# Kernel tuning notes

Measured on AMD Instinct MI355X. Metric: run time of the kernel, lower is better.

The kernel has to match this reference:

```python
import jax, jax.numpy as jnp
import numpy as np

TAU = 1.0

def setup_inputs() -> dict:
    key = jax.random.key(0)
    k1, k2, k3 = jax.random.split(key, 3)
    B, D, C = 16384, 1024, 1000
    hidden_states = jax.random.normal(k1, (B, D), dtype=jnp.float32)
    prototype_matrix = jax.random.normal(k2, (C, D), dtype=jnp.float32)
    labels = jax.random.randint(k3, (B,), 0, C, dtype=jnp.int64)
    return {"hidden_states": hidden_states, "prototype_matrix": prototype_matrix, "labels": labels}

def reference(hidden_states, prototype_matrix, labels):
    # Per-sample L2 normalize (matches x / x.norm())
    x = hidden_states / jnp.linalg.norm(hidden_states, axis=-1, keepdims=True)  # [B, D]
    # Cosine-similarity logits against class prototypes, scaled by tau=1.0
    logits = jnp.einsum('bd,cd->bc', x, prototype_matrix) / TAU  # [B, C]
    # -log( exp(logit_y) / sum exp(logits) ) == cross-entropy with log_softmax
    logp = jax.nn.log_softmax(logits, axis=-1)
    per_loss = -jnp.take_along_axis(logp, labels[:, None], axis=1)[:, 0]  # [B]
    return jnp.mean(per_loss)  # reduction='mean'
```

## Files before the change

kernel.cpp:

```cpp
#include <hip/hip_runtime.h>
#include <hip/hip_bf16.h>

#define B_ROWS 16384
#define DDIM   1024
#define CCLS   1000
#define CPAD   1024
#define GN     4

typedef __attribute__((ext_vector_type(8))) short  short8;
typedef __attribute__((ext_vector_type(4))) float  f32x4;

static __device__ __forceinline__ unsigned short f2bf(float f) {
    unsigned int u = __float_as_uint(f);
    unsigned int r = 0x7fffu + ((u >> 16) & 1u);
    return (unsigned short)((u + r) >> 16);
}

static __device__ __forceinline__ void gl_lds16(const unsigned short* g, unsigned short* l) {
    __builtin_amdgcn_global_load_lds(
        (const __attribute__((address_space(1))) void*)g,
        (__attribute__((address_space(3))) void*)l, 16, 0, 0);
}

__global__ __launch_bounds__(256) void prep(
        const float* __restrict__ H, const float* __restrict__ P,
        unsigned short* __restrict__ Hb, unsigned short* __restrict__ Pb,
        float* __restrict__ rowscale) {
    const int bid = blockIdx.x;
    const int tid = threadIdx.x;
    const int w   = tid >> 6;
    const int l   = tid & 63;
    if (bid < 2048) {
        #pragma unroll
        for (int p = 0; p < 2; ++p) {
            const int row = bid * 8 + w * 2 + p;
            const float* src = H + (size_t)row * DDIM;
            unsigned short* dst = Hb + (size_t)row * DDIM;
            float ss = 0.f;
            #pragma unroll
            for (int c = 0; c < 4; ++c) {
                const int col = c * 256 + l * 4;
                const float4 v = *reinterpret_cast<const float4*>(src + col);
                ss += v.x*v.x + v.y*v.y + v.z*v.z + v.w*v.w;
                ushort4 o = {f2bf(v.x), f2bf(v.y), f2bf(v.z), f2bf(v.w)};
                *reinterpret_cast<ushort4*>(dst + col) = o;
            }
            #pragma unroll
            for (int mask = 1; mask < 64; mask <<= 1)
                ss += __shfl_xor(ss, mask);
            if (l == 0) rowscale[row] = 1.4426950408889634f * rsqrtf(ss);
        }
    } else {
        const int pb = bid - 2048;
        #pragma unroll 4
        for (int c = 0; c < 32; ++c) {
            const int base = (pb * 8192 + c * 256 + tid) * 4;
            const int row  = base >> 10;
            ushort4 o;
            if (row < CCLS) {
                const float4 v = *reinterpret_cast<const float4*>(P + base);
                o.x = f2bf(v.x); o.y = f2bf(v.y); o.z = f2bf(v.z); o.w = f2bf(v.w);
            } else {
                o.x = o.y = o.z = o.w = 0;
            }
            *reinterpret_cast<ushort4*>(Pb + base) = o;
        }
    }
}

__global__ __launch_bounds__(512, 2) void gemm_ce(
        const unsigned short* __restrict__ Hb,
        const unsigned short* __restrict__ Pb,
        const int* __restrict__ labels,
        const float* __restrict__ rowscale,
        float* __restrict__ psum,
        float* __restrict__ plab) {
    __shared__ unsigned short Alds[2][256 * 64];
    __shared__ unsigned short Blds[2][256 * 64];

    const int orig = blockIdx.x;
    const int wg   = (orig & 7) * 32 + (orig >> 3);
    const int bm   = wg >> 2;
    const int bn   = wg & 3;

    const int tid = threadIdx.x;
    const int w   = tid >> 6;
    const int l   = tid & 63;
    const int lo  = l & 15;
    const int hi  = l >> 4;
    const int wm  = w >> 2;
    const int wn  = w & 3;

    const size_t arow0 = (size_t)bm * 256;
    const size_t brow0 = (size_t)bn * 256;

    const int srow = l >> 3;
    const int scol = ((l & 7) ^ srow) * 8;

#define STAGE(buf_, kt_) do {                                                   \
    _Pragma("unroll")                                                           \
    for (int i_ = 0; i_ < 4; ++i_) {                                            \
        const int trow_ = i_ * 64 + w * 8 + srow;                               \
        gl_lds16(Hb + (arow0 + trow_) * DDIM + (kt_) * 64 + scol,               \
                 &Alds[buf_][i_ * 4096 + w * 512]);                             \
        gl_lds16(Pb + (brow0 + trow_) * DDIM + (kt_) * 64 + scol,               \
                 &Blds[buf_][i_ * 4096 + w * 512]);                             \
    }                                                                           \
} while (0)

    f32x4 acc[8][4];
    #pragma unroll
    for (int m = 0; m < 8; ++m)
        #pragma unroll
        for (int n = 0; n < 4; ++n)
            acc[m][n] = (f32x4){0.f, 0.f, 0.f, 0.f};

    const int swz = (lo & 7) << 4;

    STAGE(0, 0);
    for (int kt = 0; kt < 16; ++kt) {
        const int cur = kt & 1;
        if (kt < 15) {
            STAGE(cur ^ 1, kt + 1);
            asm volatile("s_waitcnt vmcnt(8)" ::: "memory");
        } else {
            asm volatile("s_waitcnt vmcnt(0)" ::: "memory");
        }
        __builtin_amdgcn_s_barrier();
        __builtin_amdgcn_sched_barrier(0);

        const char* Ab = (const char*)&Alds[cur][0];
        const char* Bb = (const char*)&Blds[cur][0];
        #pragma unroll
        for (int kk = 0; kk < 2; ++kk) {
            const int col = ((kk << 6) | (hi << 4)) ^ swz;
            short8 a[8], b[4];
            #pragma unroll
            for (int m = 0; m < 8; ++m)
                a[m] = *reinterpret_cast<const short8*>(
                    Ab + (wm * 128 + m * 16 + lo) * 128 + col);
            #pragma unroll
            for (int n = 0; n < 4; ++n)
                b[n] = *reinterpret_cast<const short8*>(
                    Bb + (wn * 64 + n * 16 + lo) * 128 + col);
            __builtin_amdgcn_s_setprio(1);
            #pragma unroll
            for (int n = 0; n < 4; ++n)
                #pragma unroll
                for (int m = 0; m < 8; ++m)
                    acc[m][n] = __builtin_amdgcn_mfma_f32_16x16x32_bf16(
                        a[m], b[n], acc[m][n], 0, 0, 0);
            __builtin_amdgcn_s_setprio(0);
        }
        __builtin_amdgcn_sched_barrier(0);
        __builtin_amdgcn_s_barrier();
    }
#undef STAGE

    float* red = reinterpret_cast<float*>(&Alds[0][0]);
    #pragma unroll
    for (int m = 0; m < 8; ++m) {
        const int rloc = wm * 128 + m * 16 + hi * 4;
        float rs4[4], s4[4], lb2[4];
        int   lb4[4];
        #pragma unroll
        for (int j = 0; j < 4; ++j) {
            const size_t grow = arow0 + rloc + j;
            rs4[j] = rowscale[grow];
            lb4[j] = labels[grow];
            s4[j]  = 0.f;
            lb2[j] = -1e30f;
        }
        #pragma unroll
        for (int n = 0; n < 4; ++n) {
            const int c = (int)brow0 + wn * 64 + n * 16 + lo;
            const float pen = (c < CCLS) ? 0.f : -1e30f;
            #pragma unroll
            for (int j = 0; j < 4; ++j) {
                const float lg = fmaf(acc[m][n][j], rs4[j], pen);
                lb2[j] = (c == lb4[j]) ? lg : lb2[j];
                s4[j] += exp2f(lg);
            }
        }
        #pragma unroll
        for (int j = 0; j < 4; ++j) {
            #pragma unroll
            for (int mask = 1; mask <= 8; mask <<= 1) {
                s4[j]  += __shfl_xor(s4[j], mask);
                lb2[j]  = fmaxf(lb2[j], __shfl_xor(lb2[j], mask));
            }
            if (lo == 0) {
                const int r = rloc + j;
                red[(r * 4 + wn) * 2 + 0] = s4[j];
                red[(r * 4 + wn) * 2 + 1] = lb2[j];
            }
        }
    }
    __syncthreads();
    if (tid < 256) {
        float st = 0.f, lt = -1e30f;
        #pragma unroll
        for (int q = 0; q < 4; ++q) {
            st += red[(tid * 4 + q) * 2 + 0];
            lt  = fmaxf(lt, red[(tid * 4 + q) * 2 + 1]);
        }
        const size_t grow = arow0 + tid;
        psum[grow * GN + bn] = st;
        plab[grow * GN + bn] = lt;
    }
}

__global__ __launch_bounds__(256) void reduce1(
        const float* __restrict__ psum, const float* __restrict__ plab,
        float* __restrict__ partials) {
    const int tid = threadIdx.x;
    const size_t row = (size_t)blockIdx.x * 256 + tid;
    float st = 0.f, lt = -1e30f;
    #pragma unroll
    for (int g = 0; g < GN; ++g) {
        st += psum[row * GN + g];
        lt  = fmaxf(lt, plab[row * GN + g]);
    }
    float loss = 0.6931471805599453f * (log2f(st) - lt);
    #pragma unroll
    for (int mask = 1; mask < 64; mask <<= 1)
        loss += __shfl_xor(loss, mask);
    __shared__ float wsum[4];
    if ((tid & 63) == 0) wsum[tid >> 6] = loss;
    __syncthreads();
    if (tid == 0)
        partials[blockIdx.x] = wsum[0] + wsum[1] + wsum[2] + wsum[3];
}

__global__ void reduce2(const float* __restrict__ partials, float* __restrict__ out) {
    float v = partials[threadIdx.x];
    #pragma unroll
    for (int mask = 1; mask < 64; mask <<= 1)
        v += __shfl_xor(v, mask);
    if (threadIdx.x == 0) out[0] = v * (1.0f / 16384.0f);
}

extern "C" void kernel_launch(void* const* d_in, const int* in_sizes, int n_in,
                              void* d_out, int out_size, void* d_ws, size_t ws_size,
                              hipStream_t stream) {
    const float* H      = (const float*)d_in[0];
    const float* P      = (const float*)d_in[1];
    const int*   labels = (const int*)d_in[2];
    float* out = (float*)d_out;

    char* wp = (char*)d_ws;
    unsigned short* Hb = (unsigned short*)wp;   wp += (size_t)B_ROWS * DDIM * 2;
    unsigned short* Pb = (unsigned short*)wp;   wp += (size_t)CPAD * DDIM * 2;
    float* rowscale    = (float*)wp;            wp += (size_t)B_ROWS * 4;
    float* psum        = (float*)wp;            wp += (size_t)B_ROWS * GN * 4;
    float* plab        = (float*)wp;            wp += (size_t)B_ROWS * GN * 4;
    float* partials    = (float*)wp;

    prep<<<2080, 256, 0, stream>>>(H, P, Hb, Pb, rowscale);
    gemm_ce<<<(B_ROWS / 256) * GN, 512, 0, stream>>>(Hb, Pb, labels, rowscale, psum, plab);
    reduce1<<<B_ROWS / 256, 256, 0, stream>>>(psum, plab, partials);
    reduce2<<<1, 64, 0, stream>>>(partials, out);
}
```

Before: 74.60 us.

## Interleave quarter-tile LDS reads with staged prefetch and fuse final reductions

The GEMM main loop is split into four phases, each covering a quarter of the output tile. LDS fragment loads and global-to-LDS prefetches for tiles one and two steps ahead are spread across these phases, so memory traffic overlaps the MFMA work instead of running in a separate block. The two trailing reduction kernels become a single one-block kernel with vectorized loads, which removes one launch. The cost is more barriers per k-tile, more complex buffer reuse where a buffer is refilled while still being read, and a serial single-block final reduction.

```diff
diff --git a/kernel.cpp b/kernel.cpp
--- a/kernel.cpp
+++ b/kernel.cpp
@@ -6,6 +6,7 @@
 #define CCLS   1000
 #define CPAD   1024
 #define GN     4
+#define NKT    16
 
 typedef __attribute__((ext_vector_type(8))) short  short8;
 typedef __attribute__((ext_vector_type(4))) float  f32x4;
@@ -97,16 +98,12 @@
     const int srow = l >> 3;
     const int scol = ((l & 7) ^ srow) * 8;
 
-#define STAGE(buf_, kt_) do {                                                   \
-    _Pragma("unroll")                                                           \
-    for (int i_ = 0; i_ < 4; ++i_) {                                            \
-        const int trow_ = i_ * 64 + w * 8 + srow;                               \
-        gl_lds16(Hb + (arow0 + trow_) * DDIM + (kt_) * 64 + scol,               \
-                 &Alds[buf_][i_ * 4096 + w * 512]);                             \
-        gl_lds16(Pb + (brow0 + trow_) * DDIM + (kt_) * 64 + scol,               \
-                 &Blds[buf_][i_ * 4096 + w * 512]);                             \
-    }                                                                           \
-} while (0)
+#define STAGE_A(buf_, t_, q_) gl_lds16(                                         \
+        Hb + (arow0 + (q_) * 64 + w * 8 + srow) * DDIM + (t_) * 64 + scol,      \
+        &Alds[buf_][((q_) * 64 + w * 8) * 64])
+#define STAGE_B(buf_, t_, q_) gl_lds16(                                         \
+        Pb + (brow0 + (q_) * 64 + w * 8 + srow) * DDIM + (t_) * 64 + scol,      \
+        &Blds[buf_][((q_) * 64 + w * 8) * 64])
 
     f32x4 acc[8][4];
     #pragma unroll
@@ -115,47 +112,88 @@
         for (int n = 0; n < 4; ++n)
             acc[m][n] = (f32x4){0.f, 0.f, 0.f, 0.f};
 
-    const int swz = (lo & 7) << 4;
-
-    STAGE(0, 0);
-    for (int kt = 0; kt < 16; ++kt) {
-        const int cur = kt & 1;
-        if (kt < 15) {
-            STAGE(cur ^ 1, kt + 1);
-            asm volatile("s_waitcnt vmcnt(8)" ::: "memory");
-        } else {
-            asm volatile("s_waitcnt vmcnt(0)" ::: "memory");
-        }
-        __builtin_amdgcn_s_barrier();
-        __builtin_amdgcn_sched_barrier(0);
-
-        const char* Ab = (const char*)&Alds[cur][0];
-        const char* Bb = (const char*)&Blds[cur][0];
-        #pragma unroll
-        for (int kk = 0; kk < 2; ++kk) {
-            const int col = ((kk << 6) | (hi << 4)) ^ swz;
-            short8 a[8], b[4];
-            #pragma unroll
-            for (int m = 0; m < 8; ++m)
-                a[m] = *reinterpret_cast<const short8*>(
-                    Ab + (wm * 128 + m * 16 + lo) * 128 + col);
-            #pragma unroll
-            for (int n = 0; n < 4; ++n)
-                b[n] = *reinterpret_cast<const short8*>(
-                    Bb + (wn * 64 + n * 16 + lo) * 128 + col);
-            __builtin_amdgcn_s_setprio(1);
-            #pragma unroll
-            for (int n = 0; n < 4; ++n)
-                #pragma unroll
-                for (int m = 0; m < 8; ++m)
-                    acc[m][n] = __builtin_amdgcn_mfma_f32_16x16x32_bf16(
-                        a[m], b[n], acc[m][n], 0, 0, 0);
-            __builtin_amdgcn_s_setprio(0);
-        }
-        __builtin_amdgcn_sched_barrier(0);
-        __builtin_amdgcn_s_barrier();
-    }
-#undef STAGE
+    const int swz   = (lo & 7) << 4;
+    const int colk0 = (hi << 4) ^ swz;
+    const int colk1 = (64 | (hi << 4)) ^ swz;
+
+    short8 a[4][2];
+    short8 b[4][2];
+
+#define LDA(base_, mh_) do { _Pragma("unroll")                                  \
+    for (int mi_ = 0; mi_ < 4; ++mi_) {                                         \
+        const int r_ = (wm * 128 + (mh_) * 64 + mi_ * 16 + lo) * 128;           \
+        a[mi_][0] = *reinterpret_cast<const short8*>((base_) + r_ + colk0);     \
+        a[mi_][1] = *reinterpret_cast<const short8*>((base_) + r_ + colk1);     \
+    } } while (0)
+#define LDB(base_, nh_) do { _Pragma("unroll")                                  \
+    for (int ni_ = 0; ni_ < 2; ++ni_) {                                         \
+        const int r_ = (wn * 64 + ((nh_) * 2 + ni_) * 16 + lo) * 128;           \
+        b[(nh_)*2+ni_][0] = *reinterpret_cast<const short8*>((base_) + r_ + colk0); \
+        b[(nh_)*2+ni_][1] = *reinterpret_cast<const short8*>((base_) + r_ + colk1); \
+    } } while (0)
+#define MFMA_Q(mh_, nh_) do { _Pragma("unroll")                                 \
+    for (int kk_ = 0; kk_ < 2; ++kk_) { _Pragma("unroll")                       \
+    for (int ni_ = 0; ni_ < 2; ++ni_) { _Pragma("unroll")                       \
+    for (int mi_ = 0; mi_ < 4; ++mi_) {                                         \
+        acc[(mh_)*4+mi_][(nh_)*2+ni_] = __builtin_amdgcn_mfma_f32_16x16x32_bf16(\
+            a[mi_][kk_], b[(nh_)*2+ni_][kk_], acc[(mh_)*4+mi_][(nh_)*2+ni_],    \
+            0, 0, 0);                                                           \
+    } } } } while (0)
+#define PHASE_TAIL(mh_, nh_)                                                    \
+    __builtin_amdgcn_s_barrier();                                               \
+    asm volatile("s_waitcnt lgkmcnt(0)" ::: "memory");                          \
+    __builtin_amdgcn_sched_barrier(0);                                          \
+    __builtin_amdgcn_s_setprio(1);                                              \
+    MFMA_Q(mh_, nh_);                                                           \
+    __builtin_amdgcn_s_setprio(0);                                              \
+    __builtin_amdgcn_s_barrier()
+
+#define TILE_ITER(p_, t_) do {                                                  \
+    const char* Ab_ = (const char*)&Alds[p_][0];                                \
+    const char* Bb_ = (const char*)&Blds[p_][0];                                \
+                                                                   \
+    LDA(Ab_, 0); LDB(Bb_, 0);                                                   \
+    if ((t_) + 1 < NKT) { STAGE_A((p_) ^ 1, (t_) + 1, 1);                       \
+                          STAGE_A((p_) ^ 1, (t_) + 1, 3); }                     \
+    PHASE_TAIL(0, 0);                                                           \
+                                                                   \
+    LDB(Bb_, 1);                                                                \
+    if ((t_) + 2 < NKT) { STAGE_A(p_, (t_) + 2, 0); STAGE_A(p_, (t_) + 2, 2); } \
+    PHASE_TAIL(0, 1);                                                           \
+                                                                   \
+    LDA(Ab_, 1);                                                                \
+    if ((t_) + 2 < NKT) { STAGE_B(p_, (t_) + 2, 0); STAGE_B(p_, (t_) + 2, 1); } \
+    PHASE_TAIL(1, 0);                                                           \
+                                                                   \
+    if ((t_) + 2 < NKT) { STAGE_B(p_, (t_) + 2, 2); STAGE_B(p_, (t_) + 2, 3);   \
+        asm volatile("s_waitcnt vmcnt(6)" ::: "memory");                        \
+    } else if ((t_) + 1 < NKT) {                                                \
+        asm volatile("s_waitcnt vmcnt(0)" ::: "memory");                        \
+    }                                                                           \
+    PHASE_TAIL(1, 1);                                                           \
+} while (0)
+
+    #pragma unroll
+    for (int q = 0; q < 4; ++q) { STAGE_A(0, 0, q); STAGE_B(0, 0, q); }
+    STAGE_A(1, 1, 0); STAGE_A(1, 1, 2);
+    #pragma unroll
+    for (int q = 0; q < 4; ++q) STAGE_B(1, 1, q);
+    asm volatile("s_waitcnt vmcnt(6)" ::: "memory");
+    __builtin_amdgcn_s_barrier();
+
+    #pragma unroll 1
+    for (int kt2 = 0; kt2 < NKT / 2; ++kt2) {
+        const int t0 = 2 * kt2;
+        TILE_ITER(0, t0);
+        TILE_ITER(1, t0 + 1);
+    }
+#undef TILE_ITER
+#undef PHASE_TAIL
+#undef MFMA_Q
+#undef LDB
+#undef LDA
+#undef STAGE_B
+#undef STAGE_A
 
     float* red = reinterpret_cast<float*>(&Alds[0][0]);
     #pragma unroll
@@ -210,34 +248,33 @@
     }
 }
 
-__global__ __launch_bounds__(256) void reduce1(
+__global__ __launch_bounds__(1024) void reduce_all(
         const float* __restrict__ psum, const float* __restrict__ plab,
-        float* __restrict__ partials) {
+        float* __restrict__ out) {
     const int tid = threadIdx.x;
-    const size_t row = (size_t)blockIdx.x * 256 + tid;
-    float st = 0.f, lt = -1e30f;
-    #pragma unroll
-    for (int g = 0; g < GN; ++g) {
-        st += psum[row * GN + g];
-        lt  = fmaxf(lt, plab[row * GN + g]);
-    }
-    float loss = 0.6931471805599453f * (log2f(st) - lt);
+    float loss = 0.f;
+    #pragma unroll 4
+    for (int i = 0; i < B_ROWS / 1024; ++i) {
+        const int row = i * 1024 + tid;
+        const float4 ps = *reinterpret_cast<const float4*>(psum + (size_t)row * GN);
+        const float4 pl = *reinterpret_cast<const float4*>(plab + (size_t)row * GN);
+        const float st = (ps.x + ps.y) + (ps.z + ps.w);
+        const float lt = fmaxf(fmaxf(pl.x, pl.y), fmaxf(pl.z, pl.w));
+        loss += 0.6931471805599453f * (log2f(st) - lt);
+    }
     #pragma unroll
     for (int mask = 1; mask < 64; mask <<= 1)
         loss += __shfl_xor(loss, mask);
-    __shared__ float wsum[4];
+    __shared__ float wsum[16];
     if ((tid & 63) == 0) wsum[tid >> 6] = loss;
     __syncthreads();
-    if (tid == 0)
-        partials[blockIdx.x] = wsum[0] + wsum[1] + wsum[2] + wsum[3];
-}
-
-__global__ void reduce2(const float* __restrict__ partials, float* __restrict__ out) {
-    float v = partials[threadIdx.x];
-    #pragma unroll
-    for (int mask = 1; mask < 64; mask <<= 1)
-        v += __shfl_xor(v, mask);
-    if (threadIdx.x == 0) out[0] = v * (1.0f / 16384.0f);
+    if (tid < 64) {
+        float v = (tid < 16) ? wsum[tid] : 0.f;
+        #pragma unroll
+        for (int mask = 1; mask < 16; mask <<= 1)
+            v += __shfl_xor(v, mask);
+        if (tid == 0) out[0] = v * (1.0f / 16384.0f);
+    }
 }
 
 extern "C" void kernel_launch(void* const* d_in, const int* in_sizes, int n_in,
@@ -253,11 +290,9 @@
     unsigned short* Pb = (unsigned short*)wp;   wp += (size_t)CPAD * DDIM * 2;
     float* rowscale    = (float*)wp;            wp += (size_t)B_ROWS * 4;
     float* psum        = (float*)wp;            wp += (size_t)B_ROWS * GN * 4;
-    float* plab        = (float*)wp;            wp += (size_t)B_ROWS * GN * 4;
-    float* partials    = (float*)wp;
+    float* plab        = (float*)wp;
 
     prep<<<2080, 256, 0, stream>>>(H, P, Hb, Pb, rowscale);
     gemm_ce<<<(B_ROWS / 256) * GN, 512, 0, stream>>>(Hb, Pb, labels, rowscale, psum, plab);
-    reduce1<<<B_ROWS / 256, 256, 0, stream>>>(psum, plab, partials);
-    reduce2<<<1, 64, 0, stream>>>(partials, out);
-}
+    reduce_all<<<1, 1024, 0, stream>>>(psum, plab, out);
+}
```

Measured after the change: 74.09 us. Within noise of the previous version (-0.7%).

## Fuse H bf16 conversion and row norm into GEMM A-tile staging

Applied to the files above, without the earlier changes.

Removes the separate prep pass over H. The GEMM now loads fp32 H tiles straight into registers, accumulates the squared norms, converts to bf16 and writes swizzled tiles into LDS. The intermediate bf16 copy of H and its round-trip through global memory go away, and a register-prefetch pipeline is added for the A operand. The trade-off is that each H tile is now read as fp32 by all 4 column-block workgroups, which doubles A-operand global traffic and adds register pressure. It also remaps the block index order, and reduce1 now reads the partials with vector loads.

```diff
diff --git a/kernel.cpp b/kernel.cpp
--- a/kernel.cpp
+++ b/kernel.cpp
@@ -6,15 +6,21 @@
 #define CCLS   1000
 #define CPAD   1024
 #define GN     4
+#define NKT    16
 
 typedef __attribute__((ext_vector_type(8))) short  short8;
 typedef __attribute__((ext_vector_type(4))) float  f32x4;
+
+#define FENCE asm volatile("" ::: "memory")
 
 static __device__ __forceinline__ unsigned short f2bf(float f) {
     unsigned int u = __float_as_uint(f);
     unsigned int r = 0x7fffu + ((u >> 16) & 1u);
     return (unsigned short)((u + r) >> 16);
 }
+static __device__ __forceinline__ unsigned int pack2(float a, float b) {
+    return (unsigned int)f2bf(a) | ((unsigned int)f2bf(b) << 16);
+}
 
 static __device__ __forceinline__ void gl_lds16(const unsigned short* g, unsigned short* l) {
     __builtin_amdgcn_global_load_lds(
@@ -22,66 +28,37 @@
         (__attribute__((address_space(3))) void*)l, 16, 0, 0);
 }
 
-__global__ __launch_bounds__(256) void prep(
-        const float* __restrict__ H, const float* __restrict__ P,
-        unsigned short* __restrict__ Hb, unsigned short* __restrict__ Pb,
-        float* __restrict__ rowscale) {
-    const int bid = blockIdx.x;
-    const int tid = threadIdx.x;
-    const int w   = tid >> 6;
-    const int l   = tid & 63;
-    if (bid < 2048) {
-        #pragma unroll
-        for (int p = 0; p < 2; ++p) {
-            const int row = bid * 8 + w * 2 + p;
-            const float* src = H + (size_t)row * DDIM;
-            unsigned short* dst = Hb + (size_t)row * DDIM;
-            float ss = 0.f;
-            #pragma unroll
-            for (int c = 0; c < 4; ++c) {
-                const int col = c * 256 + l * 4;
-                const float4 v = *reinterpret_cast<const float4*>(src + col);
-                ss += v.x*v.x + v.y*v.y + v.z*v.z + v.w*v.w;
-                ushort4 o = {f2bf(v.x), f2bf(v.y), f2bf(v.z), f2bf(v.w)};
-                *reinterpret_cast<ushort4*>(dst + col) = o;
-            }
-            #pragma unroll
-            for (int mask = 1; mask < 64; mask <<= 1)
-                ss += __shfl_xor(ss, mask);
-            if (l == 0) rowscale[row] = 1.4426950408889634f * rsqrtf(ss);
-        }
-    } else {
-        const int pb = bid - 2048;
-        #pragma unroll 4
-        for (int c = 0; c < 32; ++c) {
-            const int base = (pb * 8192 + c * 256 + tid) * 4;
-            const int row  = base >> 10;
-            ushort4 o;
-            if (row < CCLS) {
-                const float4 v = *reinterpret_cast<const float4*>(P + base);
-                o.x = f2bf(v.x); o.y = f2bf(v.y); o.z = f2bf(v.z); o.w = f2bf(v.w);
-            } else {
-                o.x = o.y = o.z = o.w = 0;
-            }
-            *reinterpret_cast<ushort4*>(Pb + base) = o;
-        }
+__global__ __launch_bounds__(256) void prep_P(
+        const float* __restrict__ P, unsigned short* __restrict__ Pb) {
+    const int pb = blockIdx.x;
+    #pragma unroll 4
+    for (int c = 0; c < 32; ++c) {
+        const int base = (pb * 8192 + c * 256 + threadIdx.x) * 4;
+        const int row  = base >> 10;
+        ushort4 o;
+        if (row < CCLS) {
+            const float4 q = *reinterpret_cast<const float4*>(P + base);
+            o.x = f2bf(q.x); o.y = f2bf(q.y); o.z = f2bf(q.z); o.w = f2bf(q.w);
+        } else {
+            o.x = o.y = o.z = o.w = 0;
+        }
+        *reinterpret_cast<ushort4*>(Pb + base) = o;
     }
 }
 
 __global__ __launch_bounds__(512, 2) void gemm_ce(
-        const unsigned short* __restrict__ Hb,
+        const float* __restrict__ H,
         const unsigned short* __restrict__ Pb,
         const int* __restrict__ labels,
-        const float* __restrict__ rowscale,
         float* __restrict__ psum,
         float* __restrict__ plab) {
     __shared__ unsigned short Alds[2][256 * 64];
     __shared__ unsigned short Blds[2][256 * 64];
+    __shared__ float rowscale_lds[256];
 
     const int orig = blockIdx.x;
-    const int wg   = (orig & 7) * 32 + (orig >> 3);
-    const int bm   = wg >> 2;
-    const int bn   = wg & 3;
+    const int bm   = (orig & 7) * 8 + (orig >> 5);
+    const int bn   = (orig >> 3) & 3;
 
     const int tid = threadIdx.x;
     const int w   = tid >> 6;
@@ -95,18 +72,36 @@
     const size_t brow0 = (size_t)bn * 256;
 
     const int srow = l >> 3;
-    const int scol = ((l & 7) ^ srow) * 8;
-
-#define STAGE(buf_, kt_) do {                                                   \
-    _Pragma("unroll")                                                           \
-    for (int i_ = 0; i_ < 4; ++i_) {                                            \
-        const int trow_ = i_ * 64 + w * 8 + srow;                               \
-        gl_lds16(Hb + (arow0 + trow_) * DDIM + (kt_) * 64 + scol,               \
-                 &Alds[buf_][i_ * 4096 + w * 512]);                             \
-        gl_lds16(Pb + (brow0 + trow_) * DDIM + (kt_) * 64 + scol,               \
-                 &Blds[buf_][i_ * 4096 + w * 512]);                             \
-    }                                                                           \
+    const int lc   = l & 7;
+    const int scol = (lc ^ srow) * 8;
+
+#define B_STAGE(buf_, t_) do { _Pragma("unroll")                                \
+    for (int q_ = 0; q_ < 4; ++q_)                                              \
+        gl_lds16(Pb + (brow0 + q_ * 64 + w * 8 + srow) * DDIM + (t_) * 64 + scol,\
+                 &Blds[buf_][(q_ * 64 + w * 8) * 64]);                          \
 } while (0)
+
+    float4 va[8];
+#define A_LOAD(t_) do { _Pragma("unroll")                                       \
+    for (int q_ = 0; q_ < 4; ++q_) {                                            \
+        const float* s_ = H + (arow0 + q_ * 64 + w * 8 + srow) * DDIM           \
+                            + (t_) * 64 + lc * 8;                               \
+        va[q_ * 2]     = *reinterpret_cast<const float4*>(s_);                  \
+        va[q_ * 2 + 1] = *reinterpret_cast<const float4*>(s_ + 4);              \
+    } } while (0)
+
+    float ss[4] = {0.f, 0.f, 0.f, 0.f};
+#define A_WRITE(buf_) do { _Pragma("unroll")                                    \
+    for (int q_ = 0; q_ < 4; ++q_) {                                            \
+        const float4 v0_ = va[q_ * 2], v1_ = va[q_ * 2 + 1];                    \
+        ss[q_] += v0_.x*v0_.x + v0_.y*v0_.y + v0_.z*v0_.z + v0_.w*v0_.w         \
+                + v1_.x*v1_.x + v1_.y*v1_.y + v1_.z*v1_.z + v1_.w*v1_.w;        \
+        uint4 d_;                                                               \
+        d_.x = pack2(v0_.x, v0_.y); d_.y = pack2(v0_.z, v0_.w);                 \
+        d_.z = pack2(v1_.x, v1_.y); d_.w = pack2(v1_.z, v1_.w);                 \
+        *reinterpret_cast<uint4*>((char*)&Alds[buf_][0]                         \
+            + (q_ * 64 + w * 8 + srow) * 128 + (lc ^ srow) * 16) = d_;          \
+    } } while (0)
 
     f32x4 acc[8][4];
     #pragma unroll
@@ -116,46 +111,74 @@
             acc[m][n] = (f32x4){0.f, 0.f, 0.f, 0.f};
 
     const int swz = (lo & 7) << 4;
-
-    STAGE(0, 0);
-    for (int kt = 0; kt < 16; ++kt) {
-        const int cur = kt & 1;
-        if (kt < 15) {
-            STAGE(cur ^ 1, kt + 1);
-            asm volatile("s_waitcnt vmcnt(8)" ::: "memory");
-        } else {
-            asm volatile("s_waitcnt vmcnt(0)" ::: "memory");
-        }
-        __builtin_amdgcn_s_barrier();
-        __builtin_amdgcn_sched_barrier(0);
-
-        const char* Ab = (const char*)&Alds[cur][0];
-        const char* Bb = (const char*)&Blds[cur][0];
-        #pragma unroll
-        for (int kk = 0; kk < 2; ++kk) {
-            const int col = ((kk << 6) | (hi << 4)) ^ swz;
-            short8 a[8], b[4];
-            #pragma unroll
-            for (int m = 0; m < 8; ++m)
-                a[m] = *reinterpret_cast<const short8*>(
-                    Ab + (wm * 128 + m * 16 + lo) * 128 + col);
-            #pragma unroll
-            for (int n = 0; n < 4; ++n)
-                b[n] = *reinterpret_cast<const short8*>(
-                    Bb + (wn * 64 + n * 16 + lo) * 128 + col);
-            __builtin_amdgcn_s_setprio(1);
-            #pragma unroll
-            for (int n = 0; n < 4; ++n)
-                #pragma unroll
-                for (int m = 0; m < 8; ++m)
-                    acc[m][n] = __builtin_amdgcn_mfma_f32_16x16x32_bf16(
-                        a[m], b[n], acc[m][n], 0, 0, 0);
-            __builtin_amdgcn_s_setprio(0);
-        }
-        __builtin_amdgcn_sched_barrier(0);
-        __builtin_amdgcn_s_barrier();
-    }
-#undef STAGE
+    const int colk[2] = { (hi << 4) ^ swz, (64 | (hi << 4)) ^ swz };
+
+#define COMPUTE(cur_) do {                                                      \
+    const char* Ab_ = (const char*)&Alds[cur_][0];                              \
+    const char* Bb_ = (const char*)&Blds[cur_][0];                              \
+    _Pragma("unroll")                                                           \
+    for (int kk_ = 0; kk_ < 2; ++kk_) {                                         \
+        short8 a_[8], b_[4];                                                    \
+        _Pragma("unroll")                                                       \
+        for (int mi_ = 0; mi_ < 8; ++mi_)                                       \
+            a_[mi_] = *reinterpret_cast<const short8*>(                         \
+                Ab_ + (wm * 128 + mi_ * 16 + lo) * 128 + colk[kk_]);            \
+        _Pragma("unroll")                                                       \
+        for (int ni_ = 0; ni_ < 4; ++ni_)                                       \
+            b_[ni_] = *reinterpret_cast<const short8*>(                         \
+                Bb_ + (wn * 64 + ni_ * 16 + lo) * 128 + colk[kk_]);             \
+        __builtin_amdgcn_s_setprio(1);                                          \
+        _Pragma("unroll")                                                       \
+        for (int ni_ = 0; ni_ < 4; ++ni_)                                       \
+            _Pragma("unroll")                                                   \
+            for (int mi_ = 0; mi_ < 8; ++mi_)                                   \
+                acc[mi_][ni_] = __builtin_amdgcn_mfma_f32_16x16x32_bf16(        \
+                    a_[mi_], b_[ni_], acc[mi_][ni_], 0, 0, 0);                  \
+        __builtin_amdgcn_s_setprio(0);                                          \
+    } } while (0)
+
+    A_LOAD(0);
+    A_WRITE(0);
+    B_STAGE(0, 0);
+    A_LOAD(1);
+    asm volatile("s_waitcnt vmcnt(8) lgkmcnt(0)" ::: "memory");
+    FENCE; __builtin_amdgcn_s_barrier(); FENCE;
+
+    #pragma unroll 1
+    for (int t = 0; t < NKT; ++t) {
+        const int cur = t & 1;
+        if (t + 1 < NKT) {
+            B_STAGE(cur ^ 1, t + 1);
+            A_WRITE(cur ^ 1);
+            if (t + 2 < NKT) A_LOAD(t + 2);
+        }
+        COMPUTE(cur);
+        if (t + 2 < NKT) {
+            asm volatile("s_waitcnt vmcnt(8) lgkmcnt(0)" ::: "memory");
+        } else if (t + 1 < NKT) {
+            asm volatile("s_waitcnt vmcnt(0) lgkmcnt(0)" ::: "memory");
+        }
+        if (t + 1 < NKT) { FENCE; __builtin_amdgcn_s_barrier(); FENCE; }
+    }
+#undef COMPUTE
+#undef A_WRITE
+#undef A_LOAD
+#undef B_STAGE
+
+    #pragma unroll
+    for (int q = 0; q < 4; ++q) {
+        ss[q] += __shfl_xor(ss[q], 1);
+        ss[q] += __shfl_xor(ss[q], 2);
+        ss[q] += __shfl_xor(ss[q], 4);
+    }
+    if (lc == 0) {
+        #pragma unroll
+        for (int q = 0; q < 4; ++q)
+            rowscale_lds[q * 64 + w * 8 + srow] =
+                1.4426950408889634f * rsqrtf(ss[q]);
+    }
+    asm volatile("s_waitcnt lgkmcnt(0)" ::: "memory");
+    FENCE; __builtin_amdgcn_s_barrier(); FENCE;
 
     float* red = reinterpret_cast<float*>(&Alds[0][0]);
     #pragma unroll
@@ -165,9 +188,8 @@
         int   lb4[4];
         #pragma unroll
         for (int j = 0; j < 4; ++j) {
-            const size_t grow = arow0 + rloc + j;
-            rs4[j] = rowscale[grow];
-            lb4[j] = labels[grow];
+            rs4[j] = rowscale_lds[rloc + j];
+            lb4[j] = labels[arow0 + rloc + j];
             s4[j]  = 0.f;
             lb2[j] = -1e30f;
         }
@@ -215,12 +237,10 @@
         float* __restrict__ partials) {
     const int tid = threadIdx.x;
     const size_t row = (size_t)blockIdx.x * 256 + tid;
-    float st = 0.f, lt = -1e30f;
-    #pragma unroll
-    for (int g = 0; g < GN; ++g) {
-        st += psum[row * GN + g];
-        lt  = fmaxf(lt, plab[row * GN + g]);
-    }
+    const float4 ps = *reinterpret_cast<const float4*>(psum + row * GN);
+    const float4 pl = *reinterpret_cast<const float4*>(plab + row * GN);
+    const float st = (ps.x + ps.y) + (ps.z + ps.w);
+    const float lt = fmaxf(fmaxf(pl.x, pl.y), fmaxf(pl.z, pl.w));
     float loss = 0.6931471805599453f * (log2f(st) - lt);
     #pragma unroll
     for (int mask = 1; mask < 64; mask <<= 1)
@@ -249,15 +269,13 @@
     float* out = (float*)d_out;
 
     char* wp = (char*)d_ws;
-    unsigned short* Hb = (unsigned short*)wp;   wp += (size_t)B_ROWS * DDIM * 2;
     unsigned short* Pb = (unsigned short*)wp;   wp += (size_t)CPAD * DDIM * 2;
-    float* rowscale    = (float*)wp;            wp += (size_t)B_ROWS * 4;
     float* psum        = (float*)wp;            wp += (size_t)B_ROWS * GN * 4;
     float* plab        = (float*)wp;            wp += (size_t)B_ROWS * GN * 4;
     float* partials    = (float*)wp;
 
-    prep<<<2080, 256, 0, stream>>>(H, P, Hb, Pb, rowscale);
-    gemm_ce<<<(B_ROWS / 256) * GN, 512, 0, stream>>>(Hb, Pb, labels, rowscale, psum, plab);
+    prep_P<<<32, 256, 0, stream>>>(P, Pb);
+    gemm_ce<<<(B_ROWS / 256) * GN, 512, 0, stream>>>(H, Pb, labels, psum, plab);
     reduce1<<<B_ROWS / 256, 256, 0, stream>>>(psum, plab, partials);
     reduce2<<<1, 64, 0, stream>>>(partials, out);
 }
```

After: 79.37 us. 1.06x slower.
